# Kernel tuning notes

Measured on AMD Instinct MI355X. Metric: run time of the kernel, lower is better.

## Reference

```python
import jax, jax.numpy as jnp
import numpy as np

B = 64        # number of graphs
NPG = 4096    # nodes per graph (equal-size segments, batch ids sorted)
H = 256       # hidden_dim
C0, C1 = 256, 64  # num_clusters


def setup_inputs() -> dict:
    key = jax.random.key(0)
    ks = jax.random.split(key, 8)
    N = B * NPG
    x = jax.random.normal(ks[0], (N, H), dtype=jnp.float32)
    edge_index = jax.random.randint(ks[1], (2, N), 0, N, dtype=jnp.int64)  # unused by forward
    batch = jnp.repeat(jnp.arange(B, dtype=jnp.int64), NPG)  # sorted, equal-size segments
    s = 1.0 / np.sqrt(H)
    W0 = jax.random.uniform(ks[2], (H, C0), jnp.float32, -s, s)
    b0 = jax.random.uniform(ks[3], (C0,), jnp.float32, -s, s)
    W1 = jax.random.uniform(ks[4], (H, C1), jnp.float32, -s, s)
    b1 = jax.random.uniform(ks[5], (C1,), jnp.float32, -s, s)
    sf = 1.0 / np.sqrt(C1 * H)
    Wf = jax.random.uniform(ks[6], (C1 * H, H), jnp.float32, -sf, sf)
    bf = jax.random.uniform(ks[7], (H,), jnp.float32, -sf, sf)
    return {"x": x, "edge_index": edge_index, "batch": batch,
            "W0": W0, "b0": b0, "W1": W1, "b1": b1, "Wf": Wf, "bf": bf}


def reference(x, edge_index, batch, W0, b0, W1, b1, Wf, bf):
    # Level 0: softmax cluster assignment + per-graph segmented matmul A^T @ F.
    # batch ids are sorted with equal-size segments, so the per-graph Python
    # loop of the original collapses to a reshape + batched einsum.
    A0 = jax.nn.softmax(x @ W0 + b0, axis=-1)                      # [N, C0]
    f0 = jnp.einsum('bnc,bnh->bch',
                    A0.reshape(B, NPG, C0),
                    x.reshape(B, NPG, H)).reshape(B * C0, H)        # [B*C0, H]
    # Level 1: same pattern on pooled cluster features (C0 'nodes' per graph).
    A1 = jax.nn.softmax(f0 @ W1 + b1, axis=-1)                     # [B*C0, C1]
    f1 = jnp.einsum('bnc,bnh->bch',
                    A1.reshape(B, C0, C1),
                    f0.reshape(B, C0, H)).reshape(B, C1 * H)        # [B, C1*H]
    # Final pool: Linear -> ReLU (Dropout is identity in eval mode).
    return jax.nn.relu(f1 @ Wf + bf)                               # [B, H]
```

## Files before the change

kernel.cpp:

```cpp
#include <hip/hip_runtime.h>
#include <stdint.h>

#define NG   64
#define NPG  4096
#define HD   256
#define NC0  256
#define NC1  64
#define KSPLIT 2

typedef __attribute__((ext_vector_type(8))) short bfx8;
typedef __attribute__((ext_vector_type(4))) float fx4;

__device__ __forceinline__ unsigned short f2bf(float f) {
  union { float f; unsigned int u; } v; v.f = f;
  return (unsigned short)((v.u + 0x7FFFu + ((v.u >> 16) & 1u)) >> 16);
}
__device__ __forceinline__ unsigned int pack2(float a, float b) {
  return (unsigned int)f2bf(a) | ((unsigned int)f2bf(b) << 16);
}

#define ASYNC_COPY16(gptr, lptr) \
  __builtin_amdgcn_global_load_lds((const __attribute__((address_space(1))) unsigned int*)(gptr), \
                                   (__attribute__((address_space(3))) unsigned int*)(lptr), 16, 0, 0)

__global__ __launch_bounds__(256) void k_w0f(const float* __restrict__ W0,
                                             unsigned short* __restrict__ W0F) {
  int gid = blockIdx.x * 256 + threadIdx.x;
  int l15 = gid & 15;
  int q   = (gid >> 4) & 3;
  int ks  = (gid >> 6) & 1;
  int kc  = (gid >> 7) & 3;
  int cblk = gid >> 9;
  int c = cblk * 16 + l15;
  int kb = kc * 64 + ks * 32 + q * 8;
  unsigned int u[4];
  #pragma unroll
  for (int j = 0; j < 8; j += 2)
    u[j >> 1] = pack2(W0[(size_t)(kb + j) * 256 + c], W0[(size_t)(kb + j + 1) * 256 + c]);
  *(float4*)(W0F + (size_t)gid * 8) = *(float4*)u;
}

__global__ __launch_bounds__(256, 3) void k_assign0(
    const float* __restrict__ x, const unsigned short* __restrict__ W0F,
    const float* __restrict__ b0, unsigned short* __restrict__ A0T,
    unsigned short* __restrict__ xT, int g0) {
  __shared__ unsigned short lds_u[9216];
  __shared__ float red[64 * 4];

  int gl = blockIdx.x >> 6, nt = blockIdx.x & 63;
  int tid = threadIdx.x;
  int wn = tid >> 6, lane = tid & 63;
  int l15 = lane & 15, q = lane >> 4;

  fx4 acc[4][4];
  #pragma unroll
  for (int i = 0; i < 4; ++i)
    #pragma unroll
    for (int j = 0; j < 4; ++j) acc[i][j] = fx4{0.f, 0.f, 0.f, 0.f};

  const float* xbase = x + ((size_t)(g0 + gl) * NPG + (size_t)nt * 64) * HD;
  int snode = tid >> 2, sseg = (tid & 3) * 16;
  int sg0  = (tid & 3) * 2;
  int ssw  = (snode ^ (snode >> 4)) & 7;

  bfx8 bvc[4], bvn[4];
  #pragma unroll
  for (int ni = 0; ni < 4; ++ni)
    bvc[ni] = *(const bfx8*)(W0F + ((size_t)(((wn * 4 + ni) * 8 + 0) * 64 + lane)) * 8);

  {
    const float4* src = (const float4*)(xbase + (size_t)snode * HD + sseg);
    float4 v0 = src[0], v1 = src[1], v2 = src[2], v3 = src[3];
    float4 pv[2]; unsigned int* pu = (unsigned int*)pv;
    pu[0] = pack2(v0.x, v0.y); pu[1] = pack2(v0.z, v0.w);
    pu[2] = pack2(v1.x, v1.y); pu[3] = pack2(v1.z, v1.w);
    pu[4] = pack2(v2.x, v2.y); pu[5] = pack2(v2.z, v2.w);
    pu[6] = pack2(v3.x, v3.y); pu[7] = pack2(v3.z, v3.w);
    unsigned short* drow = &lds_u[snode << 6];
    *(float4*)(drow + (((sg0    ) ^ ssw) << 3)) = pv[0];
    *(float4*)(drow + (((sg0 + 1) ^ ssw) << 3)) = pv[1];
  }
  __syncthreads();

  for (int kc = 0; kc < 4; ++kc) {
    const unsigned short* xb = &lds_u[(kc & 1) * 4096];
    float4 v0, v1, v2, v3;
    if (kc < 3) {
      const float4* src = (const float4*)(xbase + (size_t)snode * HD + (kc + 1) * 64 + sseg);
      v0 = src[0]; v1 = src[1]; v2 = src[2]; v3 = src[3];
    }
    #pragma unroll
    for (int ks = 0; ks < 2; ++ks) {
      int g8 = kc * 2 + ks;
      if (g8 < 7) {
        #pragma unroll
        for (int ni = 0; ni < 4; ++ni)
          bvn[ni] = *(const bfx8*)(W0F + ((size_t)(((wn * 4 + ni) * 8 + g8 + 1) * 64 + lane)) * 8);
      }
      bfx8 af[4];
      #pragma unroll
      for (int mi = 0; mi < 4; ++mi) {
        int row = mi * 16 + l15;
        int slot = (ks * 4 + q) ^ ((row ^ (row >> 4)) & 7);
        af[mi] = *(const bfx8*)&xb[(row << 6) + (slot << 3)];
      }
      #pragma unroll
      for (int ni = 0; ni < 4; ++ni)
        #pragma unroll
        for (int mi = 0; mi < 4; ++mi)
          acc[mi][ni] = __builtin_amdgcn_mfma_f32_16x16x32_bf16(af[mi], bvc[ni], acc[mi][ni], 0, 0, 0);
      if (g8 < 7) {
        #pragma unroll
        for (int ni = 0; ni < 4; ++ni) bvc[ni] = bvn[ni];
      }
    }
    {
      int hl = tid >> 2, s4 = tid & 3, sgn = s4 * 16;
      int g = hl >> 3, off = hl & 7;
      unsigned int u[8];
      #pragma unroll
      for (int i = 0; i < 16; i += 2) {
        int n0 = sgn + i, n1 = n0 + 1;
        unsigned short a = xb[(n0 << 6) + ((g ^ ((n0 ^ (n0 >> 4)) & 7)) << 3) + off];
        unsigned short b = xb[(n1 << 6) + ((g ^ ((n1 ^ (n1 >> 4)) & 7)) << 3) + off];
        u[i >> 1] = (unsigned int)a | ((unsigned int)b << 16);
      }
      float4* dst = (float4*)(xT + ((size_t)(gl * 64 + nt) * HD + kc * 64 + hl) * 64 + sgn);
      dst[0] = *(float4*)&u[0];
      dst[1] = *(float4*)&u[4];
    }
    if (kc < 3) {
      float4 pv[2]; unsigned int* pu = (unsigned int*)pv;
      pu[0] = pack2(v0.x, v0.y); pu[1] = pack2(v0.z, v0.w);
      pu[2] = pack2(v1.x, v1.y); pu[3] = pack2(v1.z, v1.w);
      pu[4] = pack2(v2.x, v2.y); pu[5] = pack2(v2.z, v2.w);
      pu[6] = pack2(v3.x, v3.y); pu[7] = pack2(v3.z, v3.w);
      unsigned short* drow = &lds_u[(((kc & 1) ^ 1) * 4096) + (snode << 6)];
      *(float4*)(drow + (((sg0    ) ^ ssw) << 3)) = pv[0];
      *(float4*)(drow + (((sg0 + 1) ^ ssw) << 3)) = pv[1];
    }
    __syncthreads();
  }

  float bv4[4];
  #pragma unroll
  for (int ni = 0; ni < 4; ++ni) bv4[ni] = b0[wn * 64 + ni * 16 + l15];
  #pragma unroll
  for (int mi = 0; mi < 4; ++mi)
    #pragma unroll
    for (int ni = 0; ni < 4; ++ni)
      #pragma unroll
      for (int r = 0; r < 4; ++r) acc[mi][ni][r] += bv4[ni];

  float mrow[4][4];
  #pragma unroll
  for (int mi = 0; mi < 4; ++mi)
    #pragma unroll
    for (int r = 0; r < 4; ++r) {
      float m = fmaxf(fmaxf(acc[mi][0][r], acc[mi][1][r]), fmaxf(acc[mi][2][r], acc[mi][3][r]));
      #pragma unroll
      for (int off = 1; off < 16; off <<= 1) m = fmaxf(m, __shfl_xor(m, off));
      mrow[mi][r] = m;
    }
  if (l15 == 0) {
    #pragma unroll
    for (int mi = 0; mi < 4; ++mi)
      #pragma unroll
      for (int r = 0; r < 4; ++r)
        red[(mi * 16 + q * 4 + r) * 4 + wn] = mrow[mi][r];
  }
  __syncthreads();
  #pragma unroll
  for (int mi = 0; mi < 4; ++mi)
    #pragma unroll
    for (int r = 0; r < 4; ++r) {
      float4 rv = *(const float4*)&red[(mi * 16 + q * 4 + r) * 4];
      mrow[mi][r] = fmaxf(fmaxf(rv.x, rv.y), fmaxf(rv.z, rv.w));
    }
  __syncthreads();
  float srow[4][4];
  #pragma unroll
  for (int mi = 0; mi < 4; ++mi)
    #pragma unroll
    for (int r = 0; r < 4; ++r) {
      float s = 0.f;
      #pragma unroll
      for (int ni = 0; ni < 4; ++ni) {
        float e = __expf(acc[mi][ni][r] - mrow[mi][r]);
        acc[mi][ni][r] = e; s += e;
      }
      #pragma unroll
      for (int off = 1; off < 16; off <<= 1) s += __shfl_xor(s, off);
      srow[mi][r] = s;
    }
  if (l15 == 0) {
    #pragma unroll
    for (int mi = 0; mi < 4; ++mi)
      #pragma unroll
      for (int r = 0; r < 4; ++r)
        red[(mi * 16 + q * 4 + r) * 4 + wn] = srow[mi][r];
  }
  __syncthreads();
  #pragma unroll
  for (int mi = 0; mi < 4; ++mi)
    #pragma unroll
    for (int r = 0; r < 4; ++r) {
      float4 rv = *(const float4*)&red[(mi * 16 + q * 4 + r) * 4];
      float inv = 1.f / (rv.x + rv.y + rv.z + rv.w);
      #pragma unroll
      for (int ni = 0; ni < 4; ++ni) acc[mi][ni][r] *= inv;
    }
  __syncthreads();

  unsigned short* at = lds_u;
  unsigned short* A0Tg = A0T + (size_t)(gl * 64 + nt) * NC0 * 64;
  #pragma unroll
  for (int p = 0; p < 2; ++p) {
    if ((wn >> 1) == p) {
      int cb = (wn & 1) * 64;
      #pragma unroll
      for (int mi = 0; mi < 4; ++mi) {
        int ncol = mi * 16 + q * 4;
        #pragma unroll
        for (int ni = 0; ni < 4; ++ni) {
          int cl = cb + ni * 16 + l15;
          uint2 w;
          w.x = pack2(acc[mi][ni][0], acc[mi][ni][1]);
          w.y = pack2(acc[mi][ni][2], acc[mi][ni][3]);
          *(uint2*)(at + cl * 72 + ncol) = w;
        }
      }
    }
    __syncthreads();
    {
      int row = tid >> 1, sg2 = (tid & 1) * 32;
      const float4* s4p = (const float4*)(at + row * 72 + sg2);
      float4 a = s4p[0], b = s4p[1], c = s4p[2], d = s4p[3];
      float4* d4 = (float4*)(A0Tg + (size_t)(p * 128 + row) * 64 + sg2);
      d4[0] = a; d4[1] = b; d4[2] = c; d4[3] = d;
    }
    __syncthreads();
  }
}

__global__ __launch_bounds__(512, 2) void k_pool0(
    const unsigned short* __restrict__ A0T, const unsigned short* __restrict__ xT,
    float* __restrict__ f0p, int g0) {
  __shared__ unsigned short a_s[2][128 * 64];
  __shared__ unsigned short b_s[2][128 * 64];
  int bid = blockIdx.x;
  int gl, mt, nt, kidx;
  if (gridDim.x == 512) {
    int xcd = bid & 7, s = bid >> 3;
    int p = xcd + 8 * (s >> 2);
    gl = p & 63; kidx = p >> 6;
    int j = s & 3; mt = j >> 1; nt = j & 1;
  } else {
    nt = bid & 1; mt = (bid >> 1) & 1; kidx = (bid >> 2) & 1; gl = bid >> 3;
  }

  int tid = threadIdx.x;
  int wave = tid >> 6, lane = tid & 63;
  int wm = wave >> 2, wn = wave & 3;
  int l15 = lane & 15, q = lane >> 4;

  const int TPK = (NPG / 64) / KSPLIT;
  const unsigned short* abase = A0T + (size_t)gl * 64 * NC0 * 64 + (size_t)kidx * TPK * 16384 + (size_t)mt * 128 * 64;
  const unsigned short* bbase = xT  + (size_t)gl * 64 * HD  * 64 + (size_t)kidx * TPK * 16384 + (size_t)nt * 128 * 64;

  fx4 acc[4][2];
  #pragma unroll
  for (int i = 0; i < 4; ++i)
    #pragma unroll
    for (int j = 0; j < 2; ++j) acc[i][j] = fx4{0.f, 0.f, 0.f, 0.f};

  int srow = lane >> 3;
  int sg   = (lane & 7) ^ srow;
  size_t soff = (size_t)srow * 64 + (size_t)sg * 8;

  #pragma unroll
  for (int c = 0; c < 2; ++c) {
    size_t co = (size_t)c * 16384;
    #pragma unroll
    for (int i = 0; i < 2; ++i) {
      int r0 = wave * 16 + i * 8;
      ASYNC_COPY16(abase + co + (size_t)r0 * 64 + soff, &a_s[c][r0 * 64]);
      ASYNC_COPY16(bbase + co + (size_t)r0 * 64 + soff, &b_s[c][r0 * 64]);
    }
  }

  for (int t = 0; t < TPK; ++t) {
    int buf = t & 1;
    if (t < TPK - 1) asm volatile("s_waitcnt vmcnt(4)" ::: "memory");
    else             asm volatile("s_waitcnt vmcnt(0)" ::: "memory");
    __builtin_amdgcn_s_barrier();

    bfx8 af[2][4], bf[2][2];
    #pragma unroll
    for (int ks = 0; ks < 2; ++ks) {
      int gx = ((ks * 4 + q) ^ (l15 & 7)) << 3;
      #pragma unroll
      for (int mi = 0; mi < 4; ++mi)
        af[ks][mi] = *(const bfx8*)&a_s[buf][(wm * 64 + mi * 16 + l15) * 64 + gx];
      #pragma unroll
      for (int ni = 0; ni < 2; ++ni)
        bf[ks][ni] = *(const bfx8*)&b_s[buf][(wn * 32 + ni * 16 + l15) * 64 + gx];
    }
    asm volatile("s_waitcnt lgkmcnt(0)" ::: "memory");
    __builtin_amdgcn_s_barrier();

    if (t + 2 < TPK) {
      size_t co = (size_t)(t + 2) * 16384;
      #pragma unroll
      for (int i = 0; i < 2; ++i) {
        int r0 = wave * 16 + i * 8;
        ASYNC_COPY16(abase + co + (size_t)r0 * 64 + soff, &a_s[buf][r0 * 64]);
        ASYNC_COPY16(bbase + co + (size_t)r0 * 64 + soff, &b_s[buf][r0 * 64]);
      }
    }
    #pragma unroll
    for (int ks = 0; ks < 2; ++ks)
      #pragma unroll
      for (int ni = 0; ni < 2; ++ni)
        #pragma unroll
        for (int mi = 0; mi < 4; ++mi)
          acc[mi][ni] = __builtin_amdgcn_mfma_f32_16x16x32_bf16(af[ks][mi], bf[ks][ni], acc[mi][ni], 0, 0, 0);
  }

  float* dst = f0p + (size_t)kidx * NG * NC0 * HD
             + ((size_t)(g0 + gl) * NC0 + (size_t)mt * 128) * HD + (size_t)nt * 128;
  #pragma unroll
  for (int mi = 0; mi < 4; ++mi)
    #pragma unroll
    for (int ni = 0; ni < 2; ++ni) {
      int c = wm * 64 + mi * 16 + q * 4;
      int h = wn * 32 + ni * 16 + l15;
      #pragma unroll
      for (int r = 0; r < 4; ++r)
        dst[(size_t)(c + r) * HD + h] = acc[mi][ni][r];
    }
}

__global__ __launch_bounds__(256) void k_f0sum(float* __restrict__ f0) {
  size_t i = ((size_t)blockIdx.x * 256 + threadIdx.x) * 4;
  float4 a = *(const float4*)(f0 + i);
  float4 b = *(const float4*)(f0 + (size_t)NG * NC0 * HD + i);
  a.x += b.x; a.y += b.y; a.z += b.z; a.w += b.w;
  *(float4*)(f0 + i) = a;
}

__global__ __launch_bounds__(256) void k_assign1(
    const float* __restrict__ f0, const float* __restrict__ W1,
    const float* __restrict__ b1, float* __restrict__ A1) {
  __shared__ float w1s[256 * 64];
  int tid = threadIdx.x;
  #pragma unroll
  for (int i = 0; i < 16; ++i) {
    int off = i * 1024 + tid * 4;
    *(float4*)(w1s + off) = *(const float4*)(W1 + off);
  }
  __syncthreads();
  int lane = tid & 63;
  int rbase = blockIdx.x * 32 + (tid >> 6) * 8;
  float bias = b1[lane];
  for (int rr = 0; rr < 8; ++rr) {
    int row = rbase + rr;
    const float* fr = f0 + (size_t)row * 256;
    float acc = bias;
    for (int k = 0; k < 256; k += 4) {
      float4 fv = *(const float4*)(fr + k);
      acc += fv.x * w1s[(k    ) * 64 + lane];
      acc += fv.y * w1s[(k + 1) * 64 + lane];
      acc += fv.z * w1s[(k + 2) * 64 + lane];
      acc += fv.w * w1s[(k + 3) * 64 + lane];
    }
    float m = acc;
    #pragma unroll
    for (int off = 1; off < 64; off <<= 1) m = fmaxf(m, __shfl_xor(m, off));
    float e = __expf(acc - m);
    float s = e;
    #pragma unroll
    for (int off = 1; off < 64; off <<= 1) s += __shfl_xor(s, off);
    A1[(size_t)row * 64 + lane] = e / s;
  }
}

__global__ __launch_bounds__(1024) void k_pool1(
    const float* __restrict__ A1, const float* __restrict__ f0, float* __restrict__ f1) {
  __shared__ float part[3 * 256 * 16];
  int b = blockIdx.x >> 2, cg = blockIdx.x & 3;
  int tid = threadIdx.x;
  int c0g = tid >> 8;
  int h = tid & 255;
  const float* a1p = A1 + (size_t)b * NC0 * NC1 + cg * 16;
  const float* f0p = f0 + (size_t)b * NC0 * HD + h;
  float acc[16];
  #pragma unroll
  for (int j = 0; j < 16; ++j) acc[j] = 0.f;
  for (int c0 = c0g * 64; c0 < c0g * 64 + 64; ++c0) {
    float fv = f0p[(size_t)c0 * 256];
    #pragma unroll
    for (int j = 0; j < 16; ++j) acc[j] += a1p[c0 * 64 + j] * fv;
  }
  if (c0g > 0) {
    float* d = &part[((c0g - 1) * 256 + h) * 16];
    #pragma unroll
    for (int j = 0; j < 16; ++j) d[j] = acc[j];
  }
  __syncthreads();
  if (c0g == 0) {
    #pragma unroll
    for (int g = 0; g < 3; ++g) {
      const float* s = &part[(g * 256 + h) * 16];
      #pragma unroll
      for (int j = 0; j < 16; ++j) acc[j] += s[j];
    }
    float* d = f1 + (size_t)b * 16384 + (size_t)(cg * 16) * 256 + h;
    #pragma unroll
    for (int j = 0; j < 16; ++j) d[(size_t)j * 256] = acc[j];
  }
}

__global__ __launch_bounds__(512) void k_final_partial(
    const float* __restrict__ f1, const float* __restrict__ Wf, float* __restrict__ ot) {
  __shared__ float f1s[32 * 256];
  int ks = blockIdx.x >> 2;
  int ht = (blockIdx.x >> 1) & 1;
  int bh = blockIdx.x & 1;
  int tid = threadIdx.x;
  #pragma unroll
  for (int i = 0; i < 4; ++i) {
    int idx = i * 512 + tid;
    int bb = idx >> 6, c4 = idx & 63;
    *(float4*)(f1s + bb * 256 + c4 * 4) =
        *(const float4*)(f1 + (size_t)(bh * 32 + bb) * 16384 + (size_t)ks * 256 + c4 * 4);
  }
  __syncthreads();
  int h = ht * 128 + (tid & 127);
  int b0 = (tid >> 7) * 8;
  const float* wp = Wf + (size_t)ks * 256 * 256 + h;
  float acc[8];
  #pragma unroll
  for (int j = 0; j < 8; ++j) acc[j] = 0.f;
  for (int k = 0; k < 256; k += 4) {
    float w0 = wp[(size_t)(k    ) * 256];
    float w1 = wp[(size_t)(k + 1) * 256];
    float w2 = wp[(size_t)(k + 2) * 256];
    float w3 = wp[(size_t)(k + 3) * 256];
    #pragma unroll
    for (int j = 0; j < 8; ++j) {
      float4 fv = *(const float4*)(f1s + (b0 + j) * 256 + k);
      acc[j] += fv.x * w0 + fv.y * w1 + fv.z * w2 + fv.w * w3;
    }
  }
  #pragma unroll
  for (int j = 0; j < 8; ++j) atomicAdd(&ot[(bh * 32 + b0 + j) * 256 + h], acc[j]);
}

__global__ __launch_bounds__(256) void k_final_out(
    const float* __restrict__ ot, const float* __restrict__ bfv, float* __restrict__ out) {
  int i = blockIdx.x * 256 + threadIdx.x;
  float v = ot[i] + bfv[i & 255];
  out[i] = v > 0.f ? v : 0.f;
}

extern "C" void kernel_launch(void* const* d_in, const int* in_sizes, int n_in,
                              void* d_out, int out_size, void* d_ws, size_t ws_size,
                              hipStream_t stream) {
  const float* x   = (const float*)d_in[0];
  const float* W0  = (const float*)d_in[3];
  const float* b0  = (const float*)d_in[4];
  const float* W1  = (const float*)d_in[5];
  const float* b1  = (const float*)d_in[6];
  const float* Wf  = (const float*)d_in[7];
  const float* bfv = (const float*)d_in[8];
  float* out = (float*)d_out;
  char* ws = (char*)d_ws;

  float* f0p = (float*)ws;
  float* f0  = f0p;
  float* ot  = (float*)(ws + ((size_t)32 << 20));
  unsigned short* W0F = (unsigned short*)(ws + ((size_t)32 << 20) + 65536);
  size_t chunk_off = ((size_t)32 << 20) + 65536 + 131072;
  size_t per_graph = (size_t)4 * HD * NPG;
  size_t avail = ws_size > chunk_off ? ws_size - chunk_off : 0;
  int G = (int)(avail / per_graph);
  if (G > 64) G = 64;
  if (G < 1) G = 1;
  unsigned short* xT  = (unsigned short*)(ws + chunk_off);
  unsigned short* A0T = xT + (size_t)G * HD * NPG;
  float* f1 = (float*)xT;
  float* A1 = (float*)A0T;

  hipMemsetAsync(ot, 0, 65536, stream);
  k_w0f<<<32, 256, 0, stream>>>(W0, W0F);

  for (int g0 = 0; g0 < NG; g0 += G) {
    int gc = (NG - g0 < G) ? (NG - g0) : G;
    k_assign0<<<gc * 64, 256, 0, stream>>>(x, W0F, b0, A0T, xT, g0);
    k_pool0<<<gc * 4 * KSPLIT, 512, 0, stream>>>(A0T, xT, f0p, g0);
  }
  k_f0sum<<<4096, 256, 0, stream>>>(f0);
  k_assign1<<<512, 256, 0, stream>>>(f0, W1, b1, A1);
  k_pool1<<<256, 1024, 0, stream>>>(A1, f0, f1);
  k_final_partial<<<256, 512, 0, stream>>>(f1, Wf, ot);
  k_final_out<<<64, 256, 0, stream>>>(ot, bfv, out);
}
```

Measured before the change: 636.0 us.

## Replace split-K partial buffer and sum kernel with atomics; deepen x prefetch

The k_pool0 split-K partials are now accumulated straight into f0 with float atomicAdd after a memset, which removes the separate k_f0sum kernel and its read of two 16 MB partial buffers. In k_assign0 the x tile loads are issued two chunks ahead in registers with the k-loop fully unrolled, to hide global latency better. The cost is atomic traffic on 64K elements per block, a 16 MB memset, non-deterministic summation order, and more register pressure in k_assign0.

New measurement: 654.8 us. +3.0%, slower.

```diff
diff --git a/kernel.cpp b/kernel.cpp
--- a/kernel.cpp
+++ b/kernel.cpp
@@ -40,6 +40,19 @@
   *(float4*)(W0F + (size_t)gid * 8) = *(float4*)u;
 }
 
+#define XLOAD(dst, ck) do { \
+    const float4* _s = (const float4*)(xbase + (size_t)snode * HD + (ck) * 64 + sseg); \
+    dst[0] = _s[0]; dst[1] = _s[1]; dst[2] = _s[2]; dst[3] = _s[3]; } while (0)
+#define XWRITE(src, buf) do { \
+    float4 pv[2]; unsigned int* pu = (unsigned int*)pv; \
+    pu[0] = pack2(src[0].x, src[0].y); pu[1] = pack2(src[0].z, src[0].w); \
+    pu[2] = pack2(src[1].x, src[1].y); pu[3] = pack2(src[1].z, src[1].w); \
+    pu[4] = pack2(src[2].x, src[2].y); pu[5] = pack2(src[2].z, src[2].w); \
+    pu[6] = pack2(src[3].x, src[3].y); pu[7] = pack2(src[3].z, src[3].w); \
+    unsigned short* drow = &lds_u[(buf) * 4096 + (snode << 6)]; \
+    *(float4*)(drow + (((sg0    ) ^ ssw) << 3)) = pv[0]; \
+    *(float4*)(drow + (((sg0 + 1) ^ ssw) << 3)) = pv[1]; } while (0)
+
 __global__ __launch_bounds__(256, 3) void k_assign0(
     const float* __restrict__ x, const unsigned short* __restrict__ W0F,
     const float* __restrict__ b0, unsigned short* __restrict__ A0T,
@@ -68,27 +81,16 @@
   for (int ni = 0; ni < 4; ++ni)
     bvc[ni] = *(const bfx8*)(W0F + ((size_t)(((wn * 4 + ni) * 8 + 0) * 64 + lane)) * 8);
 
-  {
-    const float4* src = (const float4*)(xbase + (size_t)snode * HD + sseg);
-    float4 v0 = src[0], v1 = src[1], v2 = src[2], v3 = src[3];
-    float4 pv[2]; unsigned int* pu = (unsigned int*)pv;
-    pu[0] = pack2(v0.x, v0.y); pu[1] = pack2(v0.z, v0.w);
-    pu[2] = pack2(v1.x, v1.y); pu[3] = pack2(v1.z, v1.w);
-    pu[4] = pack2(v2.x, v2.y); pu[5] = pack2(v2.z, v2.w);
-    pu[6] = pack2(v3.x, v3.y); pu[7] = pack2(v3.z, v3.w);
-    unsigned short* drow = &lds_u[snode << 6];
-    *(float4*)(drow + (((sg0    ) ^ ssw) << 3)) = pv[0];
-    *(float4*)(drow + (((sg0 + 1) ^ ssw) << 3)) = pv[1];
-  }
-  __syncthreads();
-
+  float4 va[4], vb[4];
+  XLOAD(va, 0);
+  XLOAD(vb, 1);
+  XWRITE(va, 0);
+  XLOAD(va, 2);
+  __syncthreads();
+
+  #pragma unroll
   for (int kc = 0; kc < 4; ++kc) {
     const unsigned short* xb = &lds_u[(kc & 1) * 4096];
-    float4 v0, v1, v2, v3;
-    if (kc < 3) {
-      const float4* src = (const float4*)(xbase + (size_t)snode * HD + (kc + 1) * 64 + sseg);
-      v0 = src[0]; v1 = src[1]; v2 = src[2]; v3 = src[3];
-    }
     #pragma unroll
     for (int ks = 0; ks < 2; ++ks) {
       int g8 = kc * 2 + ks;
@@ -129,16 +131,9 @@
       dst[0] = *(float4*)&u[0];
       dst[1] = *(float4*)&u[4];
     }
-    if (kc < 3) {
-      float4 pv[2]; unsigned int* pu = (unsigned int*)pv;
-      pu[0] = pack2(v0.x, v0.y); pu[1] = pack2(v0.z, v0.w);
-      pu[2] = pack2(v1.x, v1.y); pu[3] = pack2(v1.z, v1.w);
-      pu[4] = pack2(v2.x, v2.y); pu[5] = pack2(v2.z, v2.w);
-      pu[6] = pack2(v3.x, v3.y); pu[7] = pack2(v3.z, v3.w);
-      unsigned short* drow = &lds_u[(((kc & 1) ^ 1) * 4096) + (snode << 6)];
-      *(float4*)(drow + (((sg0    ) ^ ssw) << 3)) = pv[0];
-      *(float4*)(drow + (((sg0 + 1) ^ ssw) << 3)) = pv[1];
-    }
+    if (kc == 0) { XWRITE(vb, 1); XLOAD(vb, 3); }
+    else if (kc == 1) { XWRITE(va, 0); }
+    else if (kc == 2) { XWRITE(vb, 1); }
     __syncthreads();
   }
 
@@ -245,7 +240,7 @@
 
 __global__ __launch_bounds__(512, 2) void k_pool0(
     const unsigned short* __restrict__ A0T, const unsigned short* __restrict__ xT,
-    float* __restrict__ f0p, int g0) {
+    float* __restrict__ f0, int g0) {
   __shared__ unsigned short a_s[2][128 * 64];
   __shared__ unsigned short b_s[2][128 * 64];
   int bid = blockIdx.x;
@@ -327,8 +322,7 @@
           acc[mi][ni] = __builtin_amdgcn_mfma_f32_16x16x32_bf16(af[ks][mi], bf[ks][ni], acc[mi][ni], 0, 0, 0);
   }
 
-  float* dst = f0p + (size_t)kidx * NG * NC0 * HD
-             + ((size_t)(g0 + gl) * NC0 + (size_t)mt * 128) * HD + (size_t)nt * 128;
+  float* dst = f0 + ((size_t)(g0 + gl) * NC0 + (size_t)mt * 128) * HD + (size_t)nt * 128;
   #pragma unroll
   for (int mi = 0; mi < 4; ++mi)
     #pragma unroll
@@ -337,16 +331,8 @@
       int h = wn * 32 + ni * 16 + l15;
       #pragma unroll
       for (int r = 0; r < 4; ++r)
-        dst[(size_t)(c + r) * HD + h] = acc[mi][ni][r];
-    }
-}
-
-__global__ __launch_bounds__(256) void k_f0sum(float* __restrict__ f0) {
-  size_t i = ((size_t)blockIdx.x * 256 + threadIdx.x) * 4;
-  float4 a = *(const float4*)(f0 + i);
-  float4 b = *(const float4*)(f0 + (size_t)NG * NC0 * HD + i);
-  a.x += b.x; a.y += b.y; a.z += b.z; a.w += b.w;
-  *(float4*)(f0 + i) = a;
+        atomicAdd(&dst[(size_t)(c + r) * HD + h], acc[mi][ni][r]);
+    }
 }
 
 __global__ __launch_bounds__(256) void k_assign1(
@@ -477,8 +463,7 @@
   float* out = (float*)d_out;
   char* ws = (char*)d_ws;
 
-  float* f0p = (float*)ws;
-  float* f0  = f0p;
+  float* f0  = (float*)ws;
   float* ot  = (float*)(ws + ((size_t)32 << 20));
   unsigned short* W0F = (unsigned short*)(ws + ((size_t)32 << 20) + 65536);
   size_t chunk_off = ((size_t)32 << 20) + 65536 + 131072;
@@ -493,14 +478,14 @@
   float* A1 = (float*)A0T;
 
   hipMemsetAsync(ot, 0, 65536, stream);
+  hipMemsetAsync(f0, 0, (size_t)NG * NC0 * HD * 4, stream);
   k_w0f<<<32, 256, 0, stream>>>(W0, W0F);
 
   for (int g0 = 0; g0 < NG; g0 += G) {
     int gc = (NG - g0 < G) ? (NG - g0) : G;
     k_assign0<<<gc * 64, 256, 0, stream>>>(x, W0F, b0, A0T, xT, g0);
-    k_pool0<<<gc * 4 * KSPLIT, 512, 0, stream>>>(A0T, xT, f0p, g0);
-  }
-  k_f0sum<<<4096, 256, 0, stream>>>(f0);
+    k_pool0<<<gc * 4 * KSPLIT, 512, 0, stream>>>(A0T, xT, f0, g0);
+  }
   k_assign1<<<512, 256, 0, stream>>>(f0, W1, b1, A1);
   k_pool1<<<256, 1024, 0, stream>>>(A1, f0, f1);
   k_final_partial<<<256, 512, 0, stream>>>(f1, Wf, ot);
```
